# Kernel optimization log

Measured on AMD Instinct MI355X. Metric: run time of the kernel, lower is better.

## Reference

```python
import jax, jax.numpy as jnp
import numpy as np

KS = 15       # erosion kernel size (ones kernel -> flat erosion = local min)
R = 60        # guided filter box-blur size
EPS = 1e-4


def _box_blur(x, r):
    # kornia box_blur: same-size mean filter, reflect padding; even kernel pads
    # (r-1)//2 before and r-1-(r-1)//2 after, per kornia _compute_padding.
    pb = (r - 1) // 2
    pa = r - 1 - pb
    xp = jnp.pad(x, ((0, 0), (0, 0), (pb, pa), (pb, pa)), mode='reflect')
    one = jnp.asarray(0.0, x.dtype)
    s = jax.lax.reduce_window(xp, one, jax.lax.add, (1, 1, r, 1), (1, 1, 1, 1), 'VALID')
    s = jax.lax.reduce_window(s, one, jax.lax.add, (1, 1, 1, r), (1, 1, 1, 1), 'VALID')
    return s / jnp.asarray(r * r, x.dtype)


def _erosion(x, k):
    # kornia flat erosion with ones kernel, geodesic border: local min over kxk
    p = k // 2
    init = jnp.asarray(jnp.inf, x.dtype)
    pad = [(0, 0), (0, 0), (p, p), (p, p)]
    e = jax.lax.reduce_window(x, init, jax.lax.min, (1, 1, k, 1), (1, 1, 1, 1), [(0, 0), (0, 0), (p, p), (0, 0)])
    e = jax.lax.reduce_window(e, init, jax.lax.min, (1, 1, 1, k), (1, 1, 1, 1), [(0, 0), (0, 0), (0, 0), (p, p)])
    return e


def setup_inputs() -> dict:
    key = jax.random.key(0)
    I = jax.random.uniform(key, (8, 3, 1080, 1920), dtype=jnp.float32)
    return {"I": I}


def reference(I) -> jnp.ndarray:
    # dark channel: per-pixel min over the 3 channels  [B,1,H,W]
    dark = jnp.min(I, axis=1, keepdims=True)
    # guided_filter_plus(dark)
    d_im = _erosion(dark, KS)
    mean_I = _box_blur(d_im, R)
    mean_p = _box_blur(dark, R)
    mean_Ip = _box_blur(d_im * dark, R)
    cov_Ip = mean_Ip - mean_I * mean_p
    mean_II = _box_blur(d_im * d_im, R)
    var_I = mean_II - mean_I * mean_I
    a = cov_Ip / (var_I + EPS)
    b = mean_p - a * mean_I
    mean_a = _box_blur(a, R)
    mean_b = _box_blur(b, R)
    q = mean_a * d_im + mean_b
    return q
```

## Files before the change

kernel.cpp:

```cpp
#include <hip/hip_runtime.h>
#include <hip/hip_fp16.h>

#define HH 1080
#define WW 1920
#define NB 8
#define HWP (HH*WW)
#define NPXs ((size_t)NB*HWP)
#define NC4 (WW/4)

#define PADI(e) ((e) + ((e) >> 5))

__device__ __forceinline__ int reflH(int y){ int r = y < 0 ? -y : y; return r >= HH ? 2*HH-2-r : r; }

__device__ __forceinline__ int xcd_swz(int p, int q){ return (p & 7)*q + (p >> 3); }

__device__ __forceinline__ unsigned pkmin(unsigned a, unsigned b){
    unsigned r; asm("v_pk_min_f16 %0, %1, %2" : "=v"(r) : "v"(a), "v"(b)); return r;
}
#define INF2 0x7C007C00u

__global__ __launch_bounds__(256) void k_dark_eh(const float* __restrict__ I,
                                                 __half* __restrict__ dark, __half* __restrict__ eh){
    __shared__ float ds[2048];
    int bid = blockIdx.x;
    int y = bid % HH;
    int b = bid / HH;
    const float* row0 = I + (size_t)b*3*HWP + (size_t)y*WW;
    size_t rb = (size_t)b*HWP + (size_t)y*WW;
    int tid = threadIdx.x;
    if (tid < 240){
        int x0 = tid*8;
        float4 c00 = *(const float4*)(row0 + x0);
        float4 c01 = *(const float4*)(row0 + x0 + 4);
        float4 c10 = *(const float4*)(row0 + HWP + x0);
        float4 c11 = *(const float4*)(row0 + HWP + x0 + 4);
        float4 c20 = *(const float4*)(row0 + 2*HWP + x0);
        float4 c21 = *(const float4*)(row0 + 2*HWP + x0 + 4);
        float m[8];
        m[0]=fminf(fminf(c00.x,c10.x),c20.x); m[1]=fminf(fminf(c00.y,c10.y),c20.y);
        m[2]=fminf(fminf(c00.z,c10.z),c20.z); m[3]=fminf(fminf(c00.w,c10.w),c20.w);
        m[4]=fminf(fminf(c01.x,c11.x),c21.x); m[5]=fminf(fminf(c01.y,c11.y),c21.y);
        m[6]=fminf(fminf(c01.z,c11.z),c21.z); m[7]=fminf(fminf(c01.w,c11.w),c21.w);
        __half2 hd[4];
        #pragma unroll
        for (int l=0;l<4;++l) hd[l] = __floats2half2_rn(m[2*l], m[2*l+1]);
        *(uint4*)(dark + rb + x0) = *(uint4*)hd;
        #pragma unroll
        for (int i=0;i<8;++i) ds[PADI(x0+7+i)] = m[i];
    } else if (tid == 240){
        for (int i=0;i<7;++i) ds[PADI(i)] = 1e30f;
    } else if (tid == 241){
        for (int i=0;i<7;++i) ds[PADI(1927+i)] = 1e30f;
    }
    __syncthreads();
    if (tid >= 240) return;
    int x0 = tid*8;
    float s[22];
    #pragma unroll
    for (int i=0;i<22;++i) s[i] = ds[PADI(x0+i)];
    float t1[21], t2[19], t4[15];
    #pragma unroll
    for (int i=0;i<21;++i) t1[i] = fminf(s[i], s[i+1]);
    #pragma unroll
    for (int i=0;i<19;++i) t2[i] = fminf(t1[i], t1[i+2]);
    #pragma unroll
    for (int i=0;i<15;++i) t4[i] = fminf(t2[i], t2[i+4]);
    __half2 ho[4];
    #pragma unroll
    for (int l=0;l<4;++l){
        float o0 = fminf(t4[2*l],   t4[2*l+7]);
        float o1 = fminf(t4[2*l+1], t4[2*l+8]);
        ho[l] = __floats2half2_rn(o0, o1);
    }
    *(uint4*)(eh + rb + x0) = *(uint4*)ho;
}

__global__ __launch_bounds__(256) void k_erosv(const __half* __restrict__ eh, __half* __restrict__ dim){
    int t = xcd_swz(blockIdx.x, 135)*256 + threadIdx.x;
    int c4 = t % NC4;
    int r  = t / NC4;
    int b  = r & 7;
    int y0 = (r >> 3) * 15;
    const __half* sp = eh  + (size_t)b*HWP + (size_t)c4*4;
    __half*       dp = dim + (size_t)b*HWP + (size_t)c4*4;
    uint2 s[15];
    #pragma unroll
    for (int j=0;j<15;++j){
        int y = y0 - 7 + j;
        if ((unsigned)y < HH) s[j] = *(const uint2*)(sp + (size_t)y*WW);
        else { s[j].x = INF2; s[j].y = INF2; }
    }
    #pragma unroll
    for (int j=13;j>=0;--j){
        s[j].x = pkmin(s[j].x, s[j+1].x); s[j].y = pkmin(s[j].y, s[j+1].y);
    }
    *(uint2*)(dp + (size_t)y0*WW) = s[0];
    uint2 P; P.x = INF2; P.y = INF2;
    #pragma unroll
    for (int j=1;j<15;++j){
        int y = y0 + 7 + j;
        uint2 nv;
        if ((unsigned)y < HH) nv = *(const uint2*)(sp + (size_t)y*WW);
        else { nv.x = INF2; nv.y = INF2; }
        P.x = pkmin(P.x, nv.x); P.y = pkmin(P.y, nv.y);
        uint2 o;
        o.x = pkmin(s[j].x, P.x); o.y = pkmin(s[j].y, P.y);
        *(uint2*)(dp + (size_t)(y0+j)*WW) = o;
    }
}

#define BT 27
__global__ __launch_bounds__(256) void k_blurv4(const __half* __restrict__ dimp, const __half* __restrict__ darkp,
                                                __half* __restrict__ m0, __half* __restrict__ m1,
                                                __half* __restrict__ m2, __half* __restrict__ m3){
    int t = xcd_swz(blockIdx.x, 75)*256 + threadIdx.x;
    int c4 = t % NC4;
    int r  = t / NC4;
    int b  = r & 7;
    int y0 = (r >> 3) * BT;
    size_t base = (size_t)b*HWP + (size_t)c4*4;
    const __half* pd = dimp + base;
    const __half* pk = darkp + base;
    float sI[4], sP[4], sIP[4], sII[4];
    #pragma unroll
    for (int i=0;i<4;++i){ sI[i]=0.f; sP[i]=0.f; sIP[i]=0.f; sII[i]=0.f; }
    auto accA = [&](int yy){
        int yr = reflH(yy);
        uint2 vd = *(const uint2*)(pd + (size_t)yr*WW);
        uint2 vk = *(const uint2*)(pk + (size_t)yr*WW);
        const __half2* hd = (const __half2*)&vd;
        const __half2* hk = (const __half2*)&vk;
        #pragma unroll
        for (int l=0;l<2;++l){
            float2 fd = __half22float2(hd[l]);
            float2 fk = __half22float2(hk[l]);
            sI[2*l]+=fd.x; sI[2*l+1]+=fd.y;
            sP[2*l]+=fk.x; sP[2*l+1]+=fk.y;
            sIP[2*l]+=fd.x*fk.x; sIP[2*l+1]+=fd.y*fk.y;
            sII[2*l]+=fd.x*fd.x; sII[2*l+1]+=fd.y*fd.y;
        }
    };
    auto accS = [&](int yy){
        int yr = reflH(yy);
        uint2 vd = *(const uint2*)(pd + (size_t)yr*WW);
        uint2 vk = *(const uint2*)(pk + (size_t)yr*WW);
        const __half2* hd = (const __half2*)&vd;
        const __half2* hk = (const __half2*)&vk;
        #pragma unroll
        for (int l=0;l<2;++l){
            float2 fd = __half22float2(hd[l]);
            float2 fk = __half22float2(hk[l]);
            sI[2*l]-=fd.x; sI[2*l+1]-=fd.y;
            sP[2*l]-=fk.x; sP[2*l+1]-=fk.y;
            sIP[2*l]-=fd.x*fk.x; sIP[2*l+1]-=fd.y*fk.y;
            sII[2*l]-=fd.x*fd.x; sII[2*l+1]-=fd.y*fd.y;
        }
    };
    const float inv = 1.0f/60.0f;
    for (int k=-29;k<=30;++k) accA(y0+k);
    auto emit = [&](int y){
        size_t off = base + (size_t)y*WW;
        __half2 h[2];
        h[0]=__floats2half2_rn(sI[0]*inv,sI[1]*inv);  h[1]=__floats2half2_rn(sI[2]*inv,sI[3]*inv);
        *(uint2*)(m0+off) = *(uint2*)h;
        h[0]=__floats2half2_rn(sP[0]*inv,sP[1]*inv);  h[1]=__floats2half2_rn(sP[2]*inv,sP[3]*inv);
        *(uint2*)(m1+off) = *(uint2*)h;
        h[0]=__floats2half2_rn(sIP[0]*inv,sIP[1]*inv); h[1]=__floats2half2_rn(sIP[2]*inv,sIP[3]*inv);
        *(uint2*)(m2+off) = *(uint2*)h;
        h[0]=__floats2half2_rn(sII[0]*inv,sII[1]*inv); h[1]=__floats2half2_rn(sII[2]*inv,sII[3]*inv);
        *(uint2*)(m3+off) = *(uint2*)h;
    };
    emit(y0);
    for (int y=y0+1; y<y0+BT; ++y){
        accA(y+30);
        accS(y-30);
        emit(y);
    }
}

__global__ __launch_bounds__(256) void k_hab(const __half* __restrict__ m0, const __half* __restrict__ m1,
                                             const __half* __restrict__ m2, const __half* __restrict__ m3,
                                             __half* __restrict__ aH, __half* __restrict__ bH){
    __shared__ float4 PA[4][256];
    __shared__ float4 PB[4][256];
    __shared__ float4 QA[2][264];
    __shared__ float4 QB[2][264];
    __shared__ float wt[4][4];
    __shared__ float wt2[2][4];

    int bid = blockIdx.x;
    int y = bid % HH;
    int b = bid / HH;
    size_t rb = (size_t)b*HWP + (size_t)y*WW;
    int tid = threadIdx.x;
    int lane = tid & 63;
    int wv = tid >> 6;

    const __half* mp0 = m0 + rb; const __half* mp1 = m1 + rb;
    const __half* mp2 = m2 + rb; const __half* mp3 = m3 + rb;

    float xv[4][8];
    int u = tid;
    if (u >= 4 && u <= 243){
        int x0 = 8*(u-4);
        const __half* mp[4] = {mp0, mp1, mp2, mp3};
        #pragma unroll
        for (int p=0;p<4;++p){
            uint4 hv = *(const uint4*)(mp[p] + x0);
            const __half2* h2 = (const __half2*)&hv;
            #pragma unroll
            for (int l=0;l<4;++l){
                float2 f = __half22float2(h2[l]);
                xv[p][2*l] = f.x; xv[p][2*l+1] = f.y;
            }
        }
    } else {
        #pragma unroll
        for (int i=0;i<8;++i){
            int s = 8*u + i;
            if (s >= 3 && s <= 1981){
                int j = s - 3;
                int x = j - 29;
                if (x < 0) x = -x;
                else if (x > 1919) x = 3838 - x;
                xv[0][i] = __half2float(mp0[x]);
                xv[1][i] = __half2float(mp1[x]);
                xv[2][i] = __half2float(mp2[x]);
                xv[3][i] = __half2float(mp3[x]);
            } else {
                xv[0][i]=0.f; xv[1][i]=0.f; xv[2][i]=0.f; xv[3][i]=0.f;
            }
        }
    }

    float ebase[4];
    #pragma unroll
    for (int p=0;p<4;++p){
        #pragma unroll
        for (int i=1;i<8;++i) xv[p][i] += xv[p][i-1];
        float v = xv[p][7];
        #pragma unroll
        for (int d=1; d<64; d<<=1){
            float tmp = __shfl_up(v, d);
            if (lane >= d) v += tmp;
        }
        ebase[p] = v - xv[p][7];
        if (lane == 63) wt[p][wv] = v;
    }
    __syncthreads();
    #pragma unroll
    for (int p=0;p<4;++p){
        float bb = ebase[p];
        if (wv > 0) bb += wt[p][0];
        if (wv > 1) bb += wt[p][1];
        if (wv > 2) bb += wt[p][2];
        #pragma unroll
        for (int i=0;i<8;++i) xv[p][i] += bb;
        if (u > 0) *((float2*)&PB[p][u-1] + 1) = make_float2(xv[p][0], xv[p][1]);
        PA[p][u] = make_float4(xv[p][2], xv[p][3], xv[p][4], xv[p][5]);
        *((float2*)&PB[p][u]) = make_float2(xv[p][6], xv[p][7]);
    }
    __syncthreads();

    float Aa[8], Bb[8];
    int t = tid;
    if (t < 240){
        const float inv = 1.0f/60.0f;
        float mm[4][8];
        #pragma unroll
        for (int p=0;p<4;++p){
            float4 loa = PA[p][t];
            float4 lob = PB[p][t];
            float4 hib = PB[p][t+7];
            float4 hia = PA[p][t+8];
            mm[p][0]=(hib.x-loa.x)*inv; mm[p][1]=(hib.y-loa.y)*inv;
            mm[p][2]=(hib.z-loa.z)*inv; mm[p][3]=(hib.w-loa.w)*inv;
            mm[p][4]=(hia.x-lob.x)*inv; mm[p][5]=(hia.y-lob.y)*inv;
            mm[p][6]=(hia.z-lob.z)*inv; mm[p][7]=(hia.w-lob.w)*inv;
        }
        #pragma unroll
        for (int i=0;i<8;++i){
            float mI=mm[0][i], mP=mm[1][i], mIp=mm[2][i], mII=mm[3][i];
            float cov = mIp - mI*mP;
            float var = mII - mI*mI;
            float a = cov / (var + 1e-4f);
            Aa[i] = a;
            Bb[i] = mP - a*mI;
        }
    } else {
        #pragma unroll
        for (int i=0;i<8;++i){ Aa[i]=0.f; Bb[i]=0.f; }
    }

    float eA, eB;
    {
        #pragma unroll
        for (int i=1;i<8;++i) Aa[i] += Aa[i-1];
        float v = Aa[7];
        #pragma unroll
        for (int d=1; d<64; d<<=1){
            float tmp = __shfl_up(v, d);
            if (lane >= d) v += tmp;
        }
        eA = v - Aa[7];
        if (lane==63) wt2[0][wv] = v;
    }
    {
        #pragma unroll
        for (int i=1;i<8;++i) Bb[i] += Bb[i-1];
        float v = Bb[7];
        #pragma unroll
        for (int d=1; d<64; d<<=1){
            float tmp = __shfl_up(v, d);
            if (lane >= d) v += tmp;
        }
        eB = v - Bb[7];
        if (lane==63) wt2[1][wv] = v;
    }
    __syncthreads();
    {
        float bb = eA;
        if (wv>0) bb += wt2[0][0];
        if (wv>1) bb += wt2[0][1];
        if (wv>2) bb += wt2[0][2];
        #pragma unroll
        for (int i=0;i<8;++i) Aa[i] += bb;
        bb = eB;
        if (wv>0) bb += wt2[1][0];
        if (wv>1) bb += wt2[1][1];
        if (wv>2) bb += wt2[1][2];
        #pragma unroll
        for (int i=0;i<8;++i) Bb[i] += bb;
    }
    *((float2*)&QB[0][t+3] + 1) = make_float2(Aa[0], Aa[1]);
    QA[0][t+4] = make_float4(Aa[2], Aa[3], Aa[4], Aa[5]);
    *((float2*)&QB[0][t+4]) = make_float2(Aa[6], Aa[7]);
    *((float2*)&QB[1][t+3] + 1) = make_float2(Bb[0], Bb[1]);
    QA[1][t+4] = make_float4(Bb[2], Bb[3], Bb[4], Bb[5]);
    *((float2*)&QB[1][t+4]) = make_float2(Bb[6], Bb[7]);
    if (tid >= 248){
        int k = tid - 248;
        float4 z4 = make_float4(0.f,0.f,0.f,0.f);
        if (k < 4){ QA[0][k] = z4; QA[1][k] = z4; }
        else if (k < 7){ QB[0][k-4] = z4; QB[1][k-4] = z4; }
        else { *((float2*)&QB[0][3]) = make_float2(0.f,0.f);
               *((float2*)&QB[1][3]) = make_float2(0.f,0.f); }
    }
    __syncthreads();
    if (t >= 240) return;

    int x0 = 8*t;
    float4 lA0 = QA[0][t];   float4 lA1 = QB[0][t];
    float4 hA0 = QB[0][t+7]; float4 hA1 = QA[0][t+8];
    float4 lB0 = QA[1][t];   float4 lB1 = QB[1][t];
    float4 hB0 = QB[1][t+7]; float4 hB1 = QA[1][t+8];
    float sA[8], sB[8];
    sA[0]=hA0.x-lA0.x; sA[1]=hA0.y-lA0.y; sA[2]=hA0.z-lA0.z; sA[3]=hA0.w-lA0.w;
    sA[4]=hA1.x-lA1.x; sA[5]=hA1.y-lA1.y; sA[6]=hA1.z-lA1.z; sA[7]=hA1.w-lA1.w;
    sB[0]=hB0.x-lB0.x; sB[1]=hB0.y-lB0.y; sB[2]=hB0.z-lB0.z; sB[3]=hB0.w-lB0.w;
    sB[4]=hB1.x-lB1.x; sB[5]=hB1.y-lB1.y; sB[6]=hB1.z-lB1.z; sB[7]=hB1.w-lB1.w;

    auto prRead = [&](int pl, int v)->float{
        int z = v + 30;
        int c = z >> 2;
        float4 f = (c & 1) ? QB[pl][c>>1] : QA[pl][c>>1];
        int w = z & 3;
        return (w==0)?f.x:((w==1)?f.y:((w==2)?f.z:f.w));
    };
    if (x0 < 29){
        #pragma unroll
        for (int i=0;i<8;++i){
            int x = x0 + i;
            if (x < 29){
                sA[i] += prRead(0, 29-x) - prRead(0, 0);
                sB[i] += prRead(1, 29-x) - prRead(1, 0);
            }
        }
    }
    if (x0 + 7 > 1889){
        #pragma unroll
        for (int i=0;i<8;++i){
            int x = x0 + i;
            if (x > 1889){
                sA[i] += prRead(0, 1918) - prRead(0, 3807-x);
                sB[i] += prRead(1, 1918) - prRead(1, 3807-x);
            }
        }
    }
    const float inv = 1.0f/60.0f;
    __half2 ha[4], hb[4];
    #pragma unroll
    for (int l=0;l<4;++l){
        ha[l] = __floats2half2_rn(sA[2*l]*inv, sA[2*l+1]*inv);
        hb[l] = __floats2half2_rn(sB[2*l]*inv, sB[2*l+1]*inv);
    }
    *(uint4*)(aH + rb + x0) = *(uint4*)ha;
    *(uint4*)(bH + rb + x0) = *(uint4*)hb;
}

__global__ __launch_bounds__(256) void k_final(const __half* __restrict__ aHp, const __half* __restrict__ bHp,
                                               const __half* __restrict__ dimp, float* __restrict__ q){
    int t = xcd_swz(blockIdx.x, 75)*256 + threadIdx.x;
    int c4 = t % NC4;
    int r  = t / NC4;
    int b  = r & 7;
    int y0 = (r >> 3) * BT;
    size_t base = (size_t)b*HWP + (size_t)c4*4;
    const __half* pa = aHp + base;
    const __half* pb = bHp + base;
    const __half* pd = dimp + base;
    float* pq = q + base;
    float sa[4], sb[4];
    #pragma unroll
    for (int i=0;i<4;++i){ sa[i]=0.f; sb[i]=0.f; }
    auto accA = [&](int yy){
        int yr = reflH(yy);
        uint2 va = *(const uint2*)(pa + (size_t)yr*WW);
        uint2 vb = *(const uint2*)(pb + (size_t)yr*WW);
        const __half2* hA = (const __half2*)&va;
        const __half2* hB = (const __half2*)&vb;
        #pragma unroll
        for (int l=0;l<2;++l){
            float2 fa = __half22float2(hA[l]);
            float2 fb = __half22float2(hB[l]);
            sa[2*l]+=fa.x; sa[2*l+1]+=fa.y;
            sb[2*l]+=fb.x; sb[2*l+1]+=fb.y;
        }
    };
    auto accS = [&](int yy){
        int yr = reflH(yy);
        uint2 va = *(const uint2*)(pa + (size_t)yr*WW);
        uint2 vb = *(const uint2*)(pb + (size_t)yr*WW);
        const __half2* hA = (const __half2*)&va;
        const __half2* hB = (const __half2*)&vb;
        #pragma unroll
        for (int l=0;l<2;++l){
            float2 fa = __half22float2(hA[l]);
            float2 fb = __half22float2(hB[l]);
            sa[2*l]-=fa.x; sa[2*l+1]-=fa.y;
            sb[2*l]-=fb.x; sb[2*l+1]-=fb.y;
        }
    };
    const float inv = 1.0f/60.0f;
    for (int k=-29;k<=30;++k) accA(y0+k);
    auto emit = [&](int y){
        uint2 vd = *(const uint2*)(pd + (size_t)y*WW);
        const __half2* hd = (const __half2*)&vd;
        float2 f0 = __half22float2(hd[0]);
        float2 f1 = __half22float2(hd[1]);
        float4 o;
        o.x = (sa[0]*inv)*f0.x + sb[0]*inv;
        o.y = (sa[1]*inv)*f0.y + sb[1]*inv;
        o.z = (sa[2]*inv)*f1.x + sb[2]*inv;
        o.w = (sa[3]*inv)*f1.y + sb[3]*inv;
        *(float4*)(pq + (size_t)y*WW) = o;
    };
    emit(y0);
    for (int y=y0+1; y<y0+BT; ++y){
        accA(y+30);
        accS(y-30);
        emit(y);
    }
}

extern "C" void kernel_launch(void* const* d_in, const int* in_sizes, int n_in,
                              void* d_out, int out_size, void* d_ws, size_t ws_size,
                              hipStream_t stream){
    const float* I = (const float*)d_in[0];
    float* qout = (float*)d_out;
    __half* ws = (__half*)d_ws;

    __half* p_dark = ws;
    __half* p_eh   = ws + NPXs;
    __half* p_dim  = ws + 2*NPXs;
    __half* p_m0   = ws + 3*NPXs;
    __half* p_m1   = ws + 4*NPXs;
    __half* p_m2   = ws + 5*NPXs;
    __half* p_m3   = ws + 6*NPXs;
    __half* p_aH   = p_dark;
    __half* p_bH   = p_eh;

    k_dark_eh<<<NB*HH, 256, 0, stream>>>(I, p_dark, p_eh);
    k_erosv  <<<1080,  256, 0, stream>>>(p_eh, p_dim);
    k_blurv4 <<<600,   256, 0, stream>>>(p_dim, p_dark, p_m0, p_m1, p_m2, p_m3);
    k_hab    <<<NB*HH, 256, 0, stream>>>(p_m0, p_m1, p_m2, p_m3, p_aH, p_bH);
    k_final  <<<600,   256, 0, stream>>>(p_aH, p_bH, p_dim, qout);
}
```

Measured before the change: 261.7 us.

## Interleave blur moment planes and a/b planes, retile vertical blurs, generalize XCD swizzle

Replaces the four separate fp16 moment planes written by the vertical blur with one interleaved [I,P,IP,II] per-pixel layout. The horizontal pass and final pass now read it with wider 16-byte loads and fewer streams. The a/b outputs are likewise interleaved into a single buffer so the final kernel issues one uint4 load per row instead of two. Vertical row tiles grow from 27 to 36 rows, cutting grid size to 450 blocks and reducing the 60-row warm-up overhead per tile at the cost of fewer blocks in flight. The XCD swizzle is rewritten to handle workgroup counts not divisible by 8.

Measured after the change: 246.3 us. 5.9% less time.

```diff
diff --git a/kernel.cpp b/kernel.cpp
--- a/kernel.cpp
+++ b/kernel.cpp
@@ -12,7 +12,12 @@
 
 __device__ __forceinline__ int reflH(int y){ int r = y < 0 ? -y : y; return r >= HH ? 2*HH-2-r : r; }
 
-__device__ __forceinline__ int xcd_swz(int p, int q){ return (p & 7)*q + (p >> 3); }
+__device__ __forceinline__ int xcd_swz(int p, int nwg){
+    int q = nwg >> 3, r = nwg & 7;
+    int x = p & 7, idx = p >> 3;
+    int start = (x < r) ? x*(q+1) : r*(q+1) + (x - r)*q;
+    return start + idx;
+}
 
 __device__ __forceinline__ unsigned pkmin(unsigned a, unsigned b){
     unsigned r; asm("v_pk_min_f16 %0, %1, %2" : "=v"(r) : "v"(a), "v"(b)); return r;
@@ -76,7 +81,7 @@
 }
 
 __global__ __launch_bounds__(256) void k_erosv(const __half* __restrict__ eh, __half* __restrict__ dim){
-    int t = xcd_swz(blockIdx.x, 135)*256 + threadIdx.x;
+    int t = xcd_swz(blockIdx.x, 1080)*256 + threadIdx.x;
     int c4 = t % NC4;
     int r  = t / NC4;
     int b  = r & 7;
@@ -109,11 +114,10 @@
     }
 }
 
-#define BT 27
+#define BT 36
 __global__ __launch_bounds__(256) void k_blurv4(const __half* __restrict__ dimp, const __half* __restrict__ darkp,
-                                                __half* __restrict__ m0, __half* __restrict__ m1,
-                                                __half* __restrict__ m2, __half* __restrict__ m3){
-    int t = xcd_swz(blockIdx.x, 75)*256 + threadIdx.x;
+                                                __half* __restrict__ mp){
+    int t = xcd_swz(blockIdx.x, 450)*256 + threadIdx.x;
     int c4 = t % NC4;
     int r  = t / NC4;
     int b  = r & 7;
@@ -159,16 +163,18 @@
     const float inv = 1.0f/60.0f;
     for (int k=-29;k<=30;++k) accA(y0+k);
     auto emit = [&](int y){
-        size_t off = base + (size_t)y*WW;
-        __half2 h[2];
-        h[0]=__floats2half2_rn(sI[0]*inv,sI[1]*inv);  h[1]=__floats2half2_rn(sI[2]*inv,sI[3]*inv);
-        *(uint2*)(m0+off) = *(uint2*)h;
-        h[0]=__floats2half2_rn(sP[0]*inv,sP[1]*inv);  h[1]=__floats2half2_rn(sP[2]*inv,sP[3]*inv);
-        *(uint2*)(m1+off) = *(uint2*)h;
-        h[0]=__floats2half2_rn(sIP[0]*inv,sIP[1]*inv); h[1]=__floats2half2_rn(sIP[2]*inv,sIP[3]*inv);
-        *(uint2*)(m2+off) = *(uint2*)h;
-        h[0]=__floats2half2_rn(sII[0]*inv,sII[1]*inv); h[1]=__floats2half2_rn(sII[2]*inv,sII[3]*inv);
-        *(uint2*)(m3+off) = *(uint2*)h;
+        size_t off = (base + (size_t)y*WW) * 4;
+        __half2 h[4];
+        h[0]=__floats2half2_rn(sI[0]*inv,  sP[0]*inv);
+        h[1]=__floats2half2_rn(sIP[0]*inv, sII[0]*inv);
+        h[2]=__floats2half2_rn(sI[1]*inv,  sP[1]*inv);
+        h[3]=__floats2half2_rn(sIP[1]*inv, sII[1]*inv);
+        *(uint4*)(mp+off) = *(uint4*)h;
+        h[0]=__floats2half2_rn(sI[2]*inv,  sP[2]*inv);
+        h[1]=__floats2half2_rn(sIP[2]*inv, sII[2]*inv);
+        h[2]=__floats2half2_rn(sI[3]*inv,  sP[3]*inv);
+        h[3]=__floats2half2_rn(sIP[3]*inv, sII[3]*inv);
+        *(uint4*)(mp+off+8) = *(uint4*)h;
     };
     emit(y0);
     for (int y=y0+1; y<y0+BT; ++y){
@@ -178,9 +184,7 @@
     }
 }
 
-__global__ __launch_bounds__(256) void k_hab(const __half* __restrict__ m0, const __half* __restrict__ m1,
-                                             const __half* __restrict__ m2, const __half* __restrict__ m3,
-                                             __half* __restrict__ aH, __half* __restrict__ bH){
+__global__ __launch_bounds__(256) void k_hab(const __half* __restrict__ mp, __half* __restrict__ abp){
     __shared__ float4 PA[4][256];
     __shared__ float4 PB[4][256];
     __shared__ float4 QA[2][264];
@@ -196,23 +200,24 @@
     int lane = tid & 63;
     int wv = tid >> 6;
 
-    const __half* mp0 = m0 + rb; const __half* mp1 = m1 + rb;
-    const __half* mp2 = m2 + rb; const __half* mp3 = m3 + rb;
+    const __half* mrow = mp + rb*4;
 
     float xv[4][8];
     int u = tid;
     if (u >= 4 && u <= 243){
         int x0 = 8*(u-4);
-        const __half* mp[4] = {mp0, mp1, mp2, mp3};
-        #pragma unroll
-        for (int p=0;p<4;++p){
-            uint4 hv = *(const uint4*)(mp[p] + x0);
-            const __half2* h2 = (const __half2*)&hv;
-            #pragma unroll
-            for (int l=0;l<4;++l){
-                float2 f = __half22float2(h2[l]);
-                xv[p][2*l] = f.x; xv[p][2*l+1] = f.y;
-            }
+        const __half* pbase = mrow + (size_t)4*x0;
+        uint4 vv[4];
+        vv[0] = *(const uint4*)(pbase);
+        vv[1] = *(const uint4*)(pbase + 8);
+        vv[2] = *(const uint4*)(pbase + 16);
+        vv[3] = *(const uint4*)(pbase + 24);
+        #pragma unroll
+        for (int i=0;i<8;++i){
+            const __half2* hh = (const __half2*)&vv[i>>1];
+            float2 fa = __half22float2(hh[(i&1)*2]);
+            float2 fb = __half22float2(hh[(i&1)*2+1]);
+            xv[0][i]=fa.x; xv[1][i]=fa.y; xv[2][i]=fb.x; xv[3][i]=fb.y;
         }
     } else {
         #pragma unroll
@@ -223,10 +228,11 @@
                 int x = j - 29;
                 if (x < 0) x = -x;
                 else if (x > 1919) x = 3838 - x;
-                xv[0][i] = __half2float(mp0[x]);
-                xv[1][i] = __half2float(mp1[x]);
-                xv[2][i] = __half2float(mp2[x]);
-                xv[3][i] = __half2float(mp3[x]);
+                uint2 u2 = *(const uint2*)(mrow + (size_t)4*x);
+                const __half2* hh = (const __half2*)&u2;
+                float2 fa = __half22float2(hh[0]);
+                float2 fb = __half22float2(hh[1]);
+                xv[0][i]=fa.x; xv[1][i]=fa.y; xv[2][i]=fb.x; xv[3][i]=fb.y;
             } else {
                 xv[0][i]=0.f; xv[1][i]=0.f; xv[2][i]=0.f; xv[3][i]=0.f;
             }
@@ -388,57 +394,46 @@
         }
     }
     const float inv = 1.0f/60.0f;
-    __half2 ha[4], hb[4];
-    #pragma unroll
-    for (int l=0;l<4;++l){
-        ha[l] = __floats2half2_rn(sA[2*l]*inv, sA[2*l+1]*inv);
-        hb[l] = __floats2half2_rn(sB[2*l]*inv, sB[2*l+1]*inv);
-    }
-    *(uint4*)(aH + rb + x0) = *(uint4*)ha;
-    *(uint4*)(bH + rb + x0) = *(uint4*)hb;
-}
-
-__global__ __launch_bounds__(256) void k_final(const __half* __restrict__ aHp, const __half* __restrict__ bHp,
+    __half2 hab[8];
+    #pragma unroll
+    for (int i=0;i<8;++i) hab[i] = __floats2half2_rn(sA[i]*inv, sB[i]*inv);
+    size_t ro = (rb + (size_t)x0) * 2;
+    *(uint4*)(abp + ro)     = *(uint4*)&hab[0];
+    *(uint4*)(abp + ro + 8) = *(uint4*)&hab[4];
+}
+
+__global__ __launch_bounds__(256) void k_final(const __half* __restrict__ abp,
                                                const __half* __restrict__ dimp, float* __restrict__ q){
-    int t = xcd_swz(blockIdx.x, 75)*256 + threadIdx.x;
+    int t = xcd_swz(blockIdx.x, 450)*256 + threadIdx.x;
     int c4 = t % NC4;
     int r  = t / NC4;
     int b  = r & 7;
     int y0 = (r >> 3) * BT;
     size_t base = (size_t)b*HWP + (size_t)c4*4;
-    const __half* pa = aHp + base;
-    const __half* pb = bHp + base;
-    const __half* pd = dimp + base;
+    const __half* pab = abp + base*2;
+    const __half* pd  = dimp + base;
     float* pq = q + base;
     float sa[4], sb[4];
     #pragma unroll
     for (int i=0;i<4;++i){ sa[i]=0.f; sb[i]=0.f; }
     auto accA = [&](int yy){
         int yr = reflH(yy);
-        uint2 va = *(const uint2*)(pa + (size_t)yr*WW);
-        uint2 vb = *(const uint2*)(pb + (size_t)yr*WW);
-        const __half2* hA = (const __half2*)&va;
-        const __half2* hB = (const __half2*)&vb;
-        #pragma unroll
-        for (int l=0;l<2;++l){
-            float2 fa = __half22float2(hA[l]);
-            float2 fb = __half22float2(hB[l]);
-            sa[2*l]+=fa.x; sa[2*l+1]+=fa.y;
-            sb[2*l]+=fb.x; sb[2*l+1]+=fb.y;
+        uint4 v = *(const uint4*)(pab + (size_t)yr*WW*2);
+        const __half2* h = (const __half2*)&v;
+        #pragma unroll
+        for (int l=0;l<4;++l){
+            float2 f = __half22float2(h[l]);
+            sa[l]+=f.x; sb[l]+=f.y;
         }
     };
     auto accS = [&](int yy){
         int yr = reflH(yy);
-        uint2 va = *(const uint2*)(pa + (size_t)yr*WW);
-        uint2 vb = *(const uint2*)(pb + (size_t)yr*WW);
-        const __half2* hA = (const __half2*)&va;
-        const __half2* hB = (const __half2*)&vb;
-        #pragma unroll
-        for (int l=0;l<2;++l){
-            float2 fa = __half22float2(hA[l]);
-            float2 fb = __half22float2(hB[l]);
-            sa[2*l]-=fa.x; sa[2*l+1]-=fa.y;
-            sb[2*l]-=fb.x; sb[2*l+1]-=fb.y;
+        uint4 v = *(const uint4*)(pab + (size_t)yr*WW*2);
+        const __half2* h = (const __half2*)&v;
+        #pragma unroll
+        for (int l=0;l<4;++l){
+            float2 f = __half22float2(h[l]);
+            sa[l]-=f.x; sb[l]-=f.y;
         }
     };
     const float inv = 1.0f/60.0f;
@@ -473,16 +468,12 @@
     __half* p_dark = ws;
     __half* p_eh   = ws + NPXs;
     __half* p_dim  = ws + 2*NPXs;
-    __half* p_m0   = ws + 3*NPXs;
-    __half* p_m1   = ws + 4*NPXs;
-    __half* p_m2   = ws + 5*NPXs;
-    __half* p_m3   = ws + 6*NPXs;
-    __half* p_aH   = p_dark;
-    __half* p_bH   = p_eh;
+    __half* p_mp   = ws + 3*NPXs;
+    __half* p_ab   = ws;
 
     k_dark_eh<<<NB*HH, 256, 0, stream>>>(I, p_dark, p_eh);
     k_erosv  <<<1080,  256, 0, stream>>>(p_eh, p_dim);
-    k_blurv4 <<<600,   256, 0, stream>>>(p_dim, p_dark, p_m0, p_m1, p_m2, p_m3);
-    k_hab    <<<NB*HH, 256, 0, stream>>>(p_m0, p_m1, p_m2, p_m3, p_aH, p_bH);
-    k_final  <<<600,   256, 0, stream>>>(p_aH, p_bH, p_dim, qout);
-}
+    k_blurv4 <<<450,   256, 0, stream>>>(p_dim, p_dark, p_mp);
+    k_hab    <<<NB*HH, 256, 0, stream>>>(p_mp, p_ab);
+    k_final  <<<450,   256, 0, stream>>>(p_ab, p_dim, qout);
+}
```
